# Performance work log

Measured on AMD Instinct MI355X. Metric: run time of the kernel, lower is better.

Reference implementation:

```python
import jax, jax.numpy as jnp
import numpy as np

B, S, HID, NH = 4, 2048, 512, 8
DH = HID // NH
NEG = -1000000.0


def setup_inputs() -> dict:
    key = jax.random.key(0)
    ks = jax.random.split(key, 8)
    scale = 1.0 / np.sqrt(HID)
    return {
        "queries": jax.random.normal(ks[0], (B, S, HID), dtype=jnp.float32),
        "keys": jax.random.normal(ks[1], (B, S, HID), dtype=jnp.float32),
        "values": jax.random.normal(ks[2], (B, S, HID), dtype=jnp.float32),
        "valid_lens": jax.random.randint(ks[3], (B,), 1, S + 1, dtype=jnp.int32),
        "Wq": jax.random.uniform(ks[4], (HID, HID), jnp.float32, -scale, scale),
        "Wk": jax.random.uniform(ks[5], (HID, HID), jnp.float32, -scale, scale),
        "Wv": jax.random.uniform(ks[6], (HID, HID), jnp.float32, -scale, scale),
        "Wo": jax.random.uniform(ks[7], (HID, HID), jnp.float32, -scale, scale),
    }


def _split_heads(x):
    # (B, S, HID) -> (B, NH, S, DH)
    return x.reshape(B, S, NH, DH).transpose(0, 2, 1, 3)


def reference(queries, keys, values, valid_lens, Wq, Wk, Wv, Wo):
    q = _split_heads(queries @ Wq.T)
    k = _split_heads(keys @ Wk.T)
    v = _split_heads(values @ Wv.T)
    scores = jnp.einsum("bhqd,bhkd->bhqk", q, k) / jnp.sqrt(jnp.float32(DH))
    # valid_lens is per-batch; mask key positions >= valid_len with -1e6 (as in sequence_mask)
    mask = jnp.arange(S)[None, :] < valid_lens[:, None]          # (B, S)
    scores = jnp.where(mask[:, None, None, :], scores, NEG)
    attn = jax.nn.softmax(scores, axis=-1)
    out = jnp.einsum("bhqk,bhkd->bhqd", attn, v)                 # (B, NH, S, DH)
    out = out.transpose(0, 2, 1, 3).reshape(B, S, HID)
    return out @ Wo.T
```

## Files before the change

kernel.cpp:

```cpp
#include <hip/hip_runtime.h>

#define B_ 4
#define S_ 2048
#define HIDN 512
#define NH 8
#define DH 64

typedef __attribute__((ext_vector_type(8))) short short8;
typedef __attribute__((ext_vector_type(4))) short short4v;
typedef __attribute__((ext_vector_type(8))) __bf16 bf16x8;
typedef __attribute__((ext_vector_type(4))) float floatx4;
typedef __attribute__((ext_vector_type(2))) unsigned uint2v;
typedef __attribute__((ext_vector_type(4))) unsigned uint4v;

__device__ inline short f2bf(float f) {
    union { float f; unsigned u; } x; x.f = f;
    unsigned r = x.u + 0x7fffu + ((x.u >> 16) & 1u);
    return (short)(r >> 16);
}

__device__ inline unsigned pack2(float a, float b) {
    unsigned ua = __builtin_bit_cast(unsigned, a) + 0x8000u;
    unsigned ub = __builtin_bit_cast(unsigned, b) + 0x8000u;
    return __builtin_amdgcn_perm(ub, ua, 0x07060302);
}

__device__ inline short8 cvt8(const float* __restrict__ p) {
    floatx4 f0 = *(const floatx4*)p;
    floatx4 f1 = *(const floatx4*)(p + 4);
    uint4v u;
    u[0] = pack2(f0[0], f0[1]); u[1] = pack2(f0[2], f0[3]);
    u[2] = pack2(f1[0], f1[1]); u[3] = pack2(f1[2], f1[3]);
    return __builtin_bit_cast(short8, u);
}

__device__ inline floatx4 mfma_s(short8 a, short8 b, floatx4 c) {
    return __builtin_amdgcn_mfma_f32_16x16x32_bf16(
        __builtin_bit_cast(bf16x8, a), __builtin_bit_cast(bf16x8, b), c, 0, 0, 0);
}

__device__ inline float vmax4(floatx4 v) {
    return fmaxf(fmaxf(v[0], v[1]), fmaxf(v[2], v[3]));
}

__global__ __launch_bounds__(256) void gemm_qkv(const float* __restrict__ xq,
                                                const float* __restrict__ xk,
                                                const float* __restrict__ xv,
                                                const float* __restrict__ wqf,
                                                const float* __restrict__ wkf,
                                                const float* __restrict__ wvf,
                                                short* __restrict__ Qh,
                                                short* __restrict__ Kh,
                                                short* __restrict__ VT) {
    const int fid = blockIdx.x;
    const int xh = fid & 7;
    const int g  = fid >> 3;
    const int xl = g / 12;
    const int rrp = g - xl * 12;
    const int y  = rrp / 3;
    const int z  = rrp - y * 3;
    const int x  = xh * 8 + xl;

    const float* X = z == 0 ? xq : (z == 1 ? xk : xv);
    const float* W = z == 0 ? wqf : (z == 1 ? wkf : wvf);
    short* dstQK = z == 0 ? Qh : Kh;

    __shared__ __align__(16) short Als[128][72];
    __shared__ __align__(16) short Bls[128][72];

    const int t = threadIdx.x;
    const int w = t >> 6, lane = t & 63, quad = lane >> 4, l16 = lane & 15;
    const int wm = (w & 1) * 64, wn = (w >> 1) * 64;
    const int m0 = x * 128, n0 = y * 128;

    floatx4 acc[4][4];
    floatx4 zero = {0.f, 0.f, 0.f, 0.f};
#pragma unroll
    for (int i = 0; i < 4; i++)
#pragma unroll
        for (int j = 0; j < 4; j++) acc[i][j] = zero;

    const int row0 = t >> 3;
    const int c8 = (t & 7) * 8;

    for (int k0 = 0; k0 < HIDN; k0 += 64) {
        __syncthreads();
#pragma unroll
        for (int rr = 0; rr < 4; rr++)
            *(short8*)&Als[row0 + rr*32][c8] =
                cvt8(&X[(m0 + row0 + rr*32) * HIDN + k0 + c8]);
#pragma unroll
        for (int rr = 0; rr < 4; rr++)
            *(short8*)&Bls[row0 + rr*32][c8] =
                cvt8(&W[(n0 + row0 + rr*32) * HIDN + k0 + c8]);
        __syncthreads();

#pragma unroll
        for (int ks = 0; ks < 2; ks++) {
            const int cq8 = (ks * 4 + quad) * 8;
            short8 a[4], b[4];
#pragma unroll
            for (int i = 0; i < 4; i++)
                a[i] = *(const short8*)&Als[wm + i*16 + l16][cq8];
#pragma unroll
            for (int j = 0; j < 4; j++)
                b[j] = *(const short8*)&Bls[wn + j*16 + l16][cq8];
#pragma unroll
            for (int i = 0; i < 4; i++)
#pragma unroll
                for (int j = 0; j < 4; j++)
                    acc[i][j] = mfma_s(a[i], b[j], acc[i][j]);
        }
    }

    if (z < 2) {
#pragma unroll
        for (int i = 0; i < 4; i++)
#pragma unroll
            for (int j = 0; j < 4; j++)
#pragma unroll
                for (int r = 0; r < 4; r++) {
                    int m = m0 + wm + i*16 + quad*4 + r;
                    int n = n0 + wn + j*16 + l16;
                    int bb = m >> 11, s = m & 2047, h = n >> 6, d = n & 63;
                    dstQK[((bb * NH + h) * S_ + s) * DH + d] = f2bf(acc[i][j][r]);
                }
    } else {
#pragma unroll
        for (int i = 0; i < 4; i++)
#pragma unroll
            for (int j = 0; j < 4; j++) {
                int s0 = m0 + wm + i*16 + quad*4;
                int n = n0 + wn + j*16 + l16;
                int bb = s0 >> 11, s = s0 & 2047, h = n >> 6, d = n & 63;
                uint2v v;
                v[0] = pack2(acc[i][j][0], acc[i][j][1]);
                v[1] = pack2(acc[i][j][2], acc[i][j][3]);
                *(uint2v*)&VT[((bb * NH + h) * DH + d) * S_ + s] = v;
            }
    }
}

__global__ __launch_bounds__(256) void gemm_out(const short* __restrict__ AO,
                                                const float* __restrict__ Wo,
                                                float* __restrict__ C) {
    const int fid = blockIdx.x;
    const int xh = fid & 7;
    const int g  = fid >> 3;
    const int xl = g >> 3;
    const int y  = g & 7;
    const int x  = xh * 8 + xl;

    __shared__ __align__(16) short Als[128][72];
    __shared__ __align__(16) short Bls[64][72];

    const int t = threadIdx.x;
    const int w = t >> 6, lane = t & 63, quad = lane >> 4, l16 = lane & 15;
    const int wm = (w & 1) * 64, wn = (w >> 1) * 32;
    const int m0 = x * 128, n0 = y * 64;

    floatx4 acc[4][2];
    floatx4 zero = {0.f, 0.f, 0.f, 0.f};
#pragma unroll
    for (int i = 0; i < 4; i++)
#pragma unroll
        for (int j = 0; j < 2; j++) acc[i][j] = zero;

    const int row0 = t >> 3;
    const int c8 = (t & 7) * 8;

    for (int k0 = 0; k0 < HIDN; k0 += 64) {
        __syncthreads();
#pragma unroll
        for (int rr = 0; rr < 4; rr++)
            *(short8*)&Als[row0 + rr*32][c8] =
                *(const short8*)&AO[(m0 + row0 + rr*32) * HIDN + k0 + c8];
#pragma unroll
        for (int rr = 0; rr < 2; rr++)
            *(short8*)&Bls[row0 + rr*32][c8] =
                cvt8(&Wo[(n0 + row0 + rr*32) * HIDN + k0 + c8]);
        __syncthreads();

#pragma unroll
        for (int ks = 0; ks < 2; ks++) {
            const int cq8 = (ks * 4 + quad) * 8;
            short8 a[4], b[2];
#pragma unroll
            for (int i = 0; i < 4; i++)
                a[i] = *(const short8*)&Als[wm + i*16 + l16][cq8];
#pragma unroll
            for (int j = 0; j < 2; j++)
                b[j] = *(const short8*)&Bls[wn + j*16 + l16][cq8];
#pragma unroll
            for (int i = 0; i < 4; i++)
#pragma unroll
                for (int j = 0; j < 2; j++)
                    acc[i][j] = mfma_s(a[i], b[j], acc[i][j]);
        }
    }

#pragma unroll
    for (int i = 0; i < 4; i++)
#pragma unroll
        for (int j = 0; j < 2; j++)
#pragma unroll
            for (int r = 0; r < 4; r++) {
                int m = m0 + wm + i*16 + quad*4 + r;
                int n = n0 + wn + j*16 + l16;
                C[m * HIDN + n] = acc[i][j][r];
            }
}

__global__ __launch_bounds__(256, 4) void attn_kernel(const short* __restrict__ Qh,
                                                      const short* __restrict__ Kh,
                                                      const short* __restrict__ VT,
                                                      const int* __restrict__ vlen,
                                                      short* __restrict__ AO) {
    __shared__ __align__(16) short Ksh[128 * 64];
    __shared__ __align__(16) short Vsh[64 * 128];
    short* Psh = Ksh;

    const int t = threadIdx.x, w = t >> 6, lane = t & 63;
    const int quad = lane >> 4, l16 = lane & 15;

    const int orig = blockIdx.x;
    const int wgid = ((orig & 7) << 7) + (orig >> 3);
    const int h = wgid >> 7;
    const int rem = wgid & 127;
    const int b = rem >> 5;
    const int qb = (rem & 31) * 64;
    const int bh = b * NH + h;
    const int vl = vlen[b];
    const int nfull = vl >> 7, rem128 = vl & 127;
    const int nt = nfull + (rem128 ? 1 : 0);

    const float SC = 0.180336879f;

    const short* qrow = &Qh[(bh * S_ + qb + w * 16 + l16) * DH];
    short8 qa0 = *(const short8*)&qrow[quad * 8];
    short8 qa1 = *(const short8*)&qrow[32 + quad * 8];

    float m_run = -1e30f, l_run = 0.f;
    floatx4 Oacc[4];
    floatx4 zero = {0.f, 0.f, 0.f, 0.f};
#pragma unroll
    for (int dt = 0; dt < 4; dt++) Oacc[dt] = zero;

    for (int kt = 0; kt < nt; kt++) {
        const int base = kt << 7;
        const bool bnd = (base + 128) > vl;
        __syncthreads();
        {
            const short* Kg = &Kh[(bh * S_ + base) * DH];
#pragma unroll
            for (int it = 0; it < 4; it++) {
                int idx = it * 256 + t;
                int row = idx >> 3, c = idx & 7;
                *(short8*)&Ksh[row * 64 + (((c ^ (row & 7))) << 3)] =
                    *(const short8*)&Kg[row * DH + (c << 3)];
            }
            const short* Vg = &VT[bh * DH * S_ + base];
#pragma unroll
            for (int it = 0; it < 4; it++) {
                int idx = it * 256 + t;
                int d = idx >> 4, c = idx & 15;
                *(short8*)&Vsh[d * 128 + (((c ^ (d & 7))) << 3)] =
                    *(const short8*)&Vg[d * S_ + (c << 3)];
            }
        }
        __syncthreads();

        floatx4 sc[8];
#pragma unroll
        for (int n = 0; n < 8; n++) {
            int krow = n * 16 + l16;
            const short* kr = &Ksh[krow * 64];
            short8 kb0 = *(const short8*)&kr[((quad ^ (krow & 7)) << 3)];
            short8 kb1 = *(const short8*)&kr[(((4 + quad) ^ (krow & 7)) << 3)];
            floatx4 s = zero;
            s = mfma_s(kb0, qa0, s);
            s = mfma_s(kb1, qa1, s);
            sc[n] = s;
        }
        __syncthreads();

        if (bnd) {
#pragma unroll
            for (int n = 0; n < 8; n++)
#pragma unroll
                for (int r = 0; r < 4; r++) {
                    int key = base + n * 16 + quad * 4 + r;
                    if (key >= vl) sc[n][r] = -1e30f;
                }
        }

        float mx = vmax4(sc[0]);
#pragma unroll
        for (int n = 1; n < 8; n++) mx = fmaxf(mx, vmax4(sc[n]));
        mx = fmaxf(mx, __shfl_xor(mx, 16));
        mx = fmaxf(mx, __shfl_xor(mx, 32));
        const float mxs = mx * SC;
        const bool norescale = __all(mxs <= m_run);
        const float mnew = norescale ? m_run : fmaxf(m_run, mxs);
        const float alpha = norescale ? 1.0f : __builtin_amdgcn_exp2f(m_run - mnew);
        m_run = mnew;
        float rs = 0.f;
#pragma unroll
        for (int n = 0; n < 8; n++)
#pragma unroll
            for (int r = 0; r < 4; r++) {
                float p = __builtin_amdgcn_exp2f(fmaf(sc[n][r], SC, -mnew));
                sc[n][r] = p;
                rs += p;
            }
        rs += __shfl_xor(rs, 16);
        rs += __shfl_xor(rs, 32);
        l_run = l_run * alpha + rs;
        if (!norescale) {
#pragma unroll
            for (int dt = 0; dt < 4; dt++)
#pragma unroll
                for (int r = 0; r < 4; r++) Oacc[dt][r] *= alpha;
        }

#pragma unroll
        for (int n = 0; n < 8; n++) {
            unsigned lo = pack2(sc[n][0], sc[n][1]);
            unsigned hi = pack2(sc[n][2], sc[n][3]);
            int c = (n << 1) + (quad >> 1);
            int idx = (w << 11) + (l16 << 7) + ((c ^ (l16 & 7)) << 3) + ((quad & 1) << 2);
            uint2v pv; pv[0] = lo; pv[1] = hi;
            *(uint2v*)&Psh[idx] = pv;
        }
        asm volatile("s_waitcnt lgkmcnt(0)" ::: "memory");
        __builtin_amdgcn_sched_barrier(0);

#pragma unroll
        for (int kk = 0; kk < 4; kk++) {
            int pc = (kk << 2) + quad;
            short8 pf = *(const short8*)&Psh[(w << 11) + (l16 << 7) + ((pc ^ (l16 & 7)) << 3)];
#pragma unroll
            for (int dt = 0; dt < 4; dt++) {
                int vrow = dt * 16 + l16;
                short8 vf = *(const short8*)&Vsh[vrow * 128 + ((pc ^ (vrow & 7)) << 3)];
                Oacc[dt] = mfma_s(vf, pf, Oacc[dt]);
            }
        }
    }

    float inv = 1.0f / l_run;
    int q = qb + w * 16 + l16;
    short* dst = &AO[(b * S_ + q) * HIDN + h * DH];
#pragma unroll
    for (int dt = 0; dt < 4; dt++) {
        uint2v v;
        v[0] = pack2(Oacc[dt][0] * inv, Oacc[dt][1] * inv);
        v[1] = pack2(Oacc[dt][2] * inv, Oacc[dt][3] * inv);
        *(uint2v*)&dst[dt * 16 + quad * 4] = v;
    }
}

extern "C" void kernel_launch(void* const* d_in, const int* in_sizes, int n_in,
                              void* d_out, int out_size, void* d_ws, size_t ws_size,
                              hipStream_t stream) {
    const float* q  = (const float*)d_in[0];
    const float* k  = (const float*)d_in[1];
    const float* v  = (const float*)d_in[2];
    const int*   vl = (const int*)d_in[3];
    const float* wq = (const float*)d_in[4];
    const float* wk = (const float*)d_in[5];
    const float* wv = (const float*)d_in[6];
    const float* wo = (const float*)d_in[7];
    float* out = (float*)d_out;

    const size_t HSZ = (size_t)B_ * NH * S_ * DH;
    short* Qh  = (short*)d_ws;
    short* Kh  = Qh + HSZ;
    short* VT  = Kh + HSZ;
    short* AO  = VT + HSZ;

    dim3 blk(256);
    gemm_qkv<<<dim3(768), blk, 0, stream>>>(q, k, v, wq, wk, wv, Qh, Kh, VT);
    attn_kernel<<<dim3(1024), blk, 0, stream>>>(Qh, Kh, VT, vl, AO);
    gemm_out<<<dim3(512), blk, 0, stream>>>(AO, wo, out);
}
```

Measured before the change: 175.7 us.

## Skip K/V projection for masked key tiles and stage QKV epilogue through LDS

K and V projection tiles whose sequence rows lie entirely beyond the batch's valid length are skipped: K tiles just return, and V tiles write zeros so the transposed V buffer stays defined. The epilogue of the QKV GEMM now stages results in shared memory and writes 16-byte coalesced rows instead of scattered 2-byte or 8-byte stores. This depends on the attention kernel never reading K beyond valid_len, and it adds LDS traffic and barriers in the epilogue.

```diff
diff --git a/kernel.cpp b/kernel.cpp
--- a/kernel.cpp
+++ b/kernel.cpp
@@ -49,6 +49,7 @@
                                                 const float* __restrict__ wqf,
                                                 const float* __restrict__ wkf,
                                                 const float* __restrict__ wvf,
+                                                const int* __restrict__ vlen,
                                                 short* __restrict__ Qh,
                                                 short* __restrict__ Kh,
                                                 short* __restrict__ VT) {
@@ -65,13 +66,36 @@
     const float* W = z == 0 ? wqf : (z == 1 ? wkf : wvf);
     short* dstQK = z == 0 ? Qh : Kh;
 
-    __shared__ __align__(16) short Als[128][72];
-    __shared__ __align__(16) short Bls[128][72];
-
     const int t = threadIdx.x;
+    const int m0 = x * 128, n0 = y * 128;
+    const int bb = m0 >> 11, sbase = m0 & 2047;
+
+    if (z >= 1) {
+        const int vl = vlen[bb];
+        if (sbase >= vl) {
+            if (z == 2) {
+#pragma unroll
+                for (int p = 0; p < 8; p++) {
+                    int idx = p * 256 + t;
+                    int nn = idx >> 4;
+                    int ch = idx & 15;
+                    int n = n0 + nn;
+                    int h = n >> 6, d = n & 63;
+                    short8 zz = {0,0,0,0,0,0,0,0};
+                    *(short8*)&VT[((bb * NH + h) * DH + d) * S_ + sbase + ch * 8] = zz;
+                }
+            }
+            return;
+        }
+    }
+
+    __shared__ __align__(16) short smem[128 * 72 * 2];
+    short (*Als)[72] = (short(*)[72])smem;
+    short (*Bls)[72] = (short(*)[72])(smem + 128 * 72);
+    short* Cls = smem;
+
     const int w = t >> 6, lane = t & 63, quad = lane >> 4, l16 = lane & 15;
     const int wm = (w & 1) * 64, wn = (w >> 1) * 64;
-    const int m0 = x * 128, n0 = y * 128;
 
     floatx4 acc[4][4];
     floatx4 zero = {0.f, 0.f, 0.f, 0.f};
@@ -113,31 +137,53 @@
         }
     }
 
+    __syncthreads();
     if (z < 2) {
 #pragma unroll
         for (int i = 0; i < 4; i++)
 #pragma unroll
-            for (int j = 0; j < 4; j++)
+            for (int j = 0; j < 4; j++) {
+                int n_l = wn + j*16 + l16;
 #pragma unroll
                 for (int r = 0; r < 4; r++) {
-                    int m = m0 + wm + i*16 + quad*4 + r;
-                    int n = n0 + wn + j*16 + l16;
-                    int bb = m >> 11, s = m & 2047, h = n >> 6, d = n & 63;
-                    dstQK[((bb * NH + h) * S_ + s) * DH + d] = f2bf(acc[i][j][r]);
+                    int m_l = wm + i*16 + quad*4 + r;
+                    Cls[m_l * 136 + n_l] = f2bf(acc[i][j][r]);
                 }
+            }
+        __syncthreads();
+#pragma unroll
+        for (int p = 0; p < 8; p++) {
+            int idx = p * 256 + t;
+            int mr = idx >> 4;
+            int ch = idx & 15;
+            short8 v = *(const short8*)&Cls[mr * 136 + ch * 8];
+            int n = n0 + ch * 8;
+            int h = n >> 6, d = n & 63;
+            *(short8*)&dstQK[((bb * NH + h) * S_ + sbase + mr) * DH + d] = v;
+        }
     } else {
 #pragma unroll
         for (int i = 0; i < 4; i++)
 #pragma unroll
             for (int j = 0; j < 4; j++) {
-                int s0 = m0 + wm + i*16 + quad*4;
-                int n = n0 + wn + j*16 + l16;
-                int bb = s0 >> 11, s = s0 & 2047, h = n >> 6, d = n & 63;
-                uint2v v;
-                v[0] = pack2(acc[i][j][0], acc[i][j][1]);
-                v[1] = pack2(acc[i][j][2], acc[i][j][3]);
-                *(uint2v*)&VT[((bb * NH + h) * DH + d) * S_ + s] = v;
-            }
+                int n_l = wn + j*16 + l16;
+                int m_l = wm + i*16 + quad*4;
+                uint2v pv;
+                pv[0] = pack2(acc[i][j][0], acc[i][j][1]);
+                pv[1] = pack2(acc[i][j][2], acc[i][j][3]);
+                *(uint2v*)&Cls[n_l * 136 + m_l] = pv;
+            }
+        __syncthreads();
+#pragma unroll
+        for (int p = 0; p < 8; p++) {
+            int idx = p * 256 + t;
+            int nn = idx >> 4;
+            int ch = idx & 15;
+            short8 v = *(const short8*)&Cls[nn * 136 + ch * 8];
+            int n = n0 + nn;
+            int h = n >> 6, d = n & 63;
+            *(short8*)&VT[((bb * NH + h) * DH + d) * S_ + sbase + ch * 8] = v;
+        }
     }
 }
 
@@ -380,7 +426,7 @@
     short* AO  = VT + HSZ;
 
     dim3 blk(256);
-    gemm_qkv<<<dim3(768), blk, 0, stream>>>(q, k, v, wq, wk, wv, Qh, Kh, VT);
+    gemm_qkv<<<dim3(768), blk, 0, stream>>>(q, k, v, wq, wk, wv, vl, Qh, Kh, VT);
     attn_kernel<<<dim3(1024), blk, 0, stream>>>(Qh, Kh, VT, vl, AO);
     gemm_out<<<dim3(512), blk, 0, stream>>>(AO, wo, out);
 }
```

New measurement: 170.9 us. -2.7%, faster.
